# Optimization experiments

Measured on AMD Instinct MI355X. Metric: run time of the kernel, lower is better.

The kernel has to match this reference:

```python
import jax, jax.numpy as jnp
import numpy as np

S, D, H = 2048, 1024, 16
DH = D // H
EPS = 1e-5


def setup_inputs() -> dict:
    key = jax.random.key(0)
    ks = jax.random.split(key, 6)
    scale = 0.02
    return {
        "inputs": jax.random.normal(ks[0], (S, D), dtype=jnp.float32),
        "ln_w": jnp.ones((D,), dtype=jnp.float32),
        "ln_b": jnp.zeros((D,), dtype=jnp.float32),
        "Wq": jax.random.normal(ks[1], (D, D), dtype=jnp.float32) * scale,
        "Wk": jax.random.normal(ks[2], (D, D), dtype=jnp.float32) * scale,
        "Wv": jax.random.normal(ks[3], (D, D), dtype=jnp.float32) * scale,
        "Wo": jax.random.normal(ks[4], (D, D), dtype=jnp.float32) * scale,
    }


def reference(inputs, ln_w, ln_b, Wq, Wk, Wv, Wo):
    # Pre-LayerNorm (per token), matching eqx.nn.LayerNorm (eps=1e-5)
    mu = jnp.mean(inputs, axis=-1, keepdims=True)
    var = jnp.var(inputs, axis=-1, keepdims=True)
    x = (inputs - mu) / jnp.sqrt(var + EPS) * ln_w + ln_b  # [S, D]

    # QKV projections (eqx Linear: y = W @ x, no bias) -> [S, H, DH]
    q = (x @ Wq.T).reshape(S, H, DH)
    k = (x @ Wk.T).reshape(S, H, DH)
    v = (x @ Wv.T).reshape(S, H, DH)

    # Scaled dot-product attention; softmax forced to full precision
    scores = jnp.einsum("shd,thd->hst", q, k) / jnp.sqrt(jnp.asarray(DH, x.dtype))
    attn = jax.nn.softmax(scores.astype(jnp.float32), axis=-1).astype(x.dtype)
    # (dropout is identity in inference mode)
    ctx = jnp.einsum("hst,thd->shd", attn, v).reshape(S, D)

    out = ctx @ Wo.T  # output projection
    # outer dropout is identity in inference mode; residual add
    return out + inputs
```

## Files before the change

### kernel.cpp

```cpp
#include <hip/hip_runtime.h>
#include <cstdint>
#include <cstddef>

typedef unsigned short u16;
typedef unsigned int u32;
typedef __attribute__((ext_vector_type(8))) short bf16x8;
typedef __attribute__((ext_vector_type(4))) short bf16x4;
typedef __attribute__((ext_vector_type(4))) float f32x4;
typedef __attribute__((ext_vector_type(4))) unsigned short u16x4;

#if __has_builtin(__builtin_amdgcn_mfma_f32_16x16x16bf16_1k)
#define MFMA16(a, b, c) __builtin_amdgcn_mfma_f32_16x16x16bf16_1k(a, b, c, 0, 0, 0)
#else
static __device__ __forceinline__ f32x4 mfma16_asm(bf16x4 a, bf16x4 b, f32x4 c) {
  asm volatile("v_mfma_f32_16x16x16_bf16 %0, %1, %2, %0\n\ts_nop 4"
               : "+v"(c) : "v"(a), "v"(b));
  return c;
}
#define MFMA16(a, b, c) mfma16_asm(a, b, c)
#endif

#if __has_builtin(__builtin_amdgcn_exp2f)
#define EXP2(x) __builtin_amdgcn_exp2f(x)
#else
#define EXP2(x) exp2f(x)
#endif

#define WAITV(N) asm volatile("s_waitcnt vmcnt(" #N ")" ::: "memory")
#define MEMFENCE() asm volatile("" ::: "memory")

__device__ __forceinline__ u16 f2b(float f) {
  union { float f; unsigned u; } un; un.f = f;
  unsigned u = un.u;
  return (u16)((u + 0x7fffu + ((u >> 16) & 1u)) >> 16);
}

__device__ __forceinline__ u32 pkbf(float a, float b) {
  union { float f; u32 u; } ua, ub; ua.f = a; ub.f = b;
  return ((ua.u + 0x8000u) >> 16) | (((ub.u + 0x8000u) >> 16) << 16);
}

__device__ __forceinline__ void gload_lds16(const u16* g, u16* l) {
  __builtin_amdgcn_global_load_lds(
      (const __attribute__((address_space(1))) void*)g,
      (__attribute__((address_space(3))) void*)l, 16, 0, 0);
}

__device__ __forceinline__ void gemm128x128(
    const u16* __restrict__ A, const u16* __restrict__ B,
    u16* smA, u16* smB, int bm, int bn,
    float* outf, u16* outb, const float* __restrict__ resid, int ostride)
{
  const int tid = threadIdx.x;
  const int wave = tid >> 6, lane = tid & 63;
  const int quad = lane >> 4, l16 = lane & 15;
  const int wm = wave >> 1, wn = wave & 1;

  f32x4 acc[4][4];
  const f32x4 zero4 = {0.f, 0.f, 0.f, 0.f};
#pragma unroll
  for (int i = 0; i < 4; i++)
#pragma unroll
    for (int j = 0; j < 4; j++) acc[i][j] = zero4;

  const u16* Ab = A + (size_t)(bm * 128) * 1024;
  const u16* Bb = B + (size_t)(bn * 128) * 1024;

#define PSTAGE(buf, k0)                                                          \
  {                                                                              \
    _Pragma("unroll")                                                            \
    for (int i = 0; i < 4; i++) {                                                \
      const int idx = i * 256 + tid;                                             \
      const int row = idx >> 3, sl = idx & 7;                                    \
      const int g = (sl ^ (row & 7)) * 8;                                        \
      gload_lds16(Ab + (size_t)row * 1024 + (k0) + g,                            \
                  smA + (buf) * 8192 + (size_t)(i * 256 + wave * 64) * 8);       \
      gload_lds16(Bb + (size_t)row * 1024 + (k0) + g,                            \
                  smB + (buf) * 8192 + (size_t)(i * 256 + wave * 64) * 8);       \
    }                                                                            \
  }

  PSTAGE(0, 0);
  for (int t = 0; t < 16; t++) {
    const int cur = t & 1;
    if (t < 15) {
      PSTAGE(cur ^ 1, (t + 1) * 64);
      WAITV(8);
    } else {
      WAITV(0);
    }
    __builtin_amdgcn_s_barrier();
    const u16* sa = smA + cur * 8192;
    const u16* sb = smB + cur * 8192;
#pragma unroll
    for (int ks = 0; ks < 2; ks++) {
      const int swz = ((ks * 4 + quad) ^ (l16 & 7)) * 8;
      bf16x8 afr[4], bfr[4];
#pragma unroll
      for (int mt = 0; mt < 4; mt++)
        afr[mt] = *(const bf16x8*)(sa + (wm * 64 + mt * 16 + l16) * 64 + swz);
#pragma unroll
      for (int nt = 0; nt < 4; nt++)
        bfr[nt] = *(const bf16x8*)(sb + (wn * 64 + nt * 16 + l16) * 64 + swz);
      __builtin_amdgcn_s_setprio(1);
#pragma unroll
      for (int mt = 0; mt < 4; mt++)
#pragma unroll
        for (int nt = 0; nt < 4; nt++)
          acc[mt][nt] = __builtin_amdgcn_mfma_f32_16x16x32_bf16(afr[mt], bfr[nt], acc[mt][nt], 0, 0, 0);
      __builtin_amdgcn_s_setprio(0);
    }
    MEMFENCE();
    __builtin_amdgcn_s_barrier();
  }
#undef PSTAGE

#pragma unroll
  for (int mt = 0; mt < 4; mt++)
#pragma unroll
    for (int nt = 0; nt < 4; nt++)
#pragma unroll
      for (int r = 0; r < 4; r++) {
        const int row = bm * 128 + wm * 64 + mt * 16 + quad * 4 + r;
        const int col = bn * 128 + wn * 64 + nt * 16 + l16;
        if (outb) outb[(size_t)row * ostride + col] = f2b(acc[mt][nt][r]);
        else outf[(size_t)row * ostride + col] =
                 acc[mt][nt][r] + resid[(size_t)row * ostride + col];
      }
}

__global__ __launch_bounds__(256, 2) void proj_k(
    const u16* __restrict__ xb, const u16* __restrict__ Wb,
    u16* __restrict__ qkbuf, u16* __restrict__ vTb)
{
  __shared__ u16 smA[2 * 128 * 64];
  __shared__ u16 smB[2 * 128 * 64];
  int b = blockIdx.x;
  const u16 *A, *B; u16* o; int bm, bn;
  if (b < 256) {
    const int c = b & 7, i = b >> 3;
    bm = ((c >> 2) << 3) | (i & 7);
    bn = ((c & 3) << 2) | (i >> 3);
    A = xb; B = Wb; o = qkbuf;
  } else {
    b -= 256;
    const int c = b & 7, i = b >> 3;
    bm = i & 7;
    bn = (c << 1) | (i >> 3);
    A = Wb + (size_t)2 * (1 << 20); B = xb; o = vTb;
  }
  gemm128x128(A, B, smA, smB, bm, bn, nullptr, o, nullptr, 2048);
}

__global__ __launch_bounds__(256, 2) void out_k(
    const u16* __restrict__ ctxb, const u16* __restrict__ Wob,
    float* __restrict__ out, const float* __restrict__ x)
{
  __shared__ u16 smA[2 * 128 * 64];
  __shared__ u16 smB[2 * 128 * 64];
  const int b = blockIdx.x;
  const int c = b & 7, i = b >> 3;
  const int bm = ((c >> 2) << 3) | (i & 7);
  const int bn = ((c & 3) << 1) | (i >> 3);
  gemm128x128(ctxb, Wob, smA, smB, bm, bn, out, nullptr, x, 1024);
}

__global__ __launch_bounds__(256) void pre_k(
    const float* __restrict__ x, const float* __restrict__ lnw, const float* __restrict__ lnb,
    const float* __restrict__ w0, const float* __restrict__ w1,
    const float* __restrict__ w2, const float* __restrict__ w3,
    u16* __restrict__ xb, u16* __restrict__ Wb)
{
  const int b = blockIdx.x;
  const int tid = threadIdx.x;
  if (b < 2048) {
    const int s = b;
    const float4 v = ((const float4*)(x + (size_t)s * 1024))[tid];
    float sum = v.x + v.y + v.z + v.w;
    float sq  = v.x * v.x + v.y * v.y + v.z * v.z + v.w * v.w;
#pragma unroll
    for (int off = 32; off >= 1; off >>= 1) {
      sum += __shfl_down(sum, off);
      sq  += __shfl_down(sq, off);
    }
    __shared__ float sS[4], sQ[4];
    const int wave = tid >> 6, lane = tid & 63;
    if (lane == 0) { sS[wave] = sum; sQ[wave] = sq; }
    __syncthreads();
    const float ts = sS[0] + sS[1] + sS[2] + sS[3];
    const float tq = sQ[0] + sQ[1] + sQ[2] + sQ[3];
    const float mu = ts * (1.0f / 1024.0f);
    const float var = tq * (1.0f / 1024.0f) - mu * mu;
    const float rstd = rsqrtf(var + 1e-5f);
    const float4 wv = ((const float4*)lnw)[tid];
    const float4 bv = ((const float4*)lnb)[tid];
    u16x4 o;
    o[0] = f2b((v.x - mu) * rstd * wv.x + bv.x);
    o[1] = f2b((v.y - mu) * rstd * wv.y + bv.y);
    o[2] = f2b((v.z - mu) * rstd * wv.z + bv.z);
    o[3] = f2b((v.w - mu) * rstd * wv.w + bv.w);
    *(u16x4*)(xb + (size_t)s * 1024 + tid * 4) = o;
  } else {
    const unsigned i = (unsigned)(b - 2048) * 1024u + tid * 4u;
    const unsigned NW = 1u << 20;
    const float* src; unsigned loc; float sc;
    if (i < NW)            { src = w0; loc = i;           sc = 0.18033688f; }
    else if (i < 2u * NW)  { src = w1; loc = i - NW;      sc = 1.0f; }
    else if (i < 3u * NW)  { src = w2; loc = i - 2u * NW; sc = 1.0f; }
    else                   { src = w3; loc = i - 3u * NW; sc = 1.0f; }
    const float4 v = *(const float4*)(src + loc);
    u16x4 r;
    r[0] = f2b(v.x * sc); r[1] = f2b(v.y * sc); r[2] = f2b(v.z * sc); r[3] = f2b(v.w * sc);
    *(u16x4*)(Wb + i) = r;
  }
}

__global__ __launch_bounds__(256, 2) void attn_k(
    const u16* __restrict__ qkbuf,
    const u16* __restrict__ vT,
    u16* __restrict__ ctx)
{
  const int bid = blockIdx.x;
  const int work = (bid & 7) * 64 + (bid >> 3);
  const int h = work >> 5;
  const int q0 = (work & 31) * 64;
  __shared__ __align__(16) unsigned char arena[65536];
  u16* kvbuf = (u16*)arena;
  const int tid = threadIdx.x;
  const int wave = tid >> 6, lane = tid & 63;
  const int quad = lane >> 4, l16 = lane & 15;
  const int a7 = l16 & 7;
  const u16* kg = qkbuf + 1024;

  bf16x8 qf[4][2];
#pragma unroll
  for (int s = 0; s < 4; s++)
#pragma unroll
    for (int ks = 0; ks < 2; ks++)
      qf[s][ks] = *(const bf16x8*)(qkbuf + (size_t)(q0 + s * 16 + l16) * 2048 + h * 64 + ks * 32 + quad * 8);

  const f32x4 zero4 = {0.f, 0.f, 0.f, 0.f};
  f32x4 Oacc[4][4];
#pragma unroll
  for (int s = 0; s < 4; s++)
#pragma unroll
    for (int dt = 0; dt < 4; dt++) Oacc[s][dt] = zero4;
  float lacc[4] = {0.f, 0.f, 0.f, 0.f};

#define STAGE(T, bf)                                                                     \
  {                                                                                      \
    _Pragma("unroll")                                                                    \
    for (int i = 0; i < 4; i++) {                                                        \
      const int idx = (wave * 4 + i) * 64 + lane;                                        \
      const int kt = idx >> 3, kc = (idx & 7) ^ (kt & 7);                                \
      gload_lds16(kg + (size_t)((T) * 128 + kt) * 2048 + h * 64 + kc * 8,                \
                  kvbuf + (bf) * 16384 + (size_t)(wave * 4 + i) * 512);                  \
      const int vd = idx >> 4, vc = (idx & 15) ^ (vd & 7);                               \
      gload_lds16(vT + (size_t)(h * 64 + vd) * 2048 + (T) * 128 + vc * 8,                \
                  kvbuf + (bf) * 16384 + 8192 + (size_t)(wave * 4 + i) * 512);           \
    }                                                                                    \
  }

  STAGE(0, 0);

  for (int T = 0; T < 16; T++) {
    const int bf = T & 1;
    if (T + 1 < 16) {
      STAGE(T + 1, 1 - bf);
      WAITV(8);
    } else {
      WAITV(0);
    }
    __builtin_amdgcn_s_barrier();
    const u16* kb = kvbuf + bf * 16384;
    const u16* vb = kb + 8192;

    f32x4 st[2][4];
#pragma unroll
    for (int ntl = 0; ntl < 2; ntl++) {
      const int nt = wave * 2 + ntl;
      const u16* kr = kb + (nt * 16 + l16) * 64;
      const bf16x8 ka0 = *(const bf16x8*)(kr + (quad ^ a7) * 8);
      const bf16x8 ka1 = *(const bf16x8*)(kr + ((4 + quad) ^ a7) * 8);
      __builtin_amdgcn_s_setprio(1);
#pragma unroll
      for (int s = 0; s < 4; s++) {
        f32x4 t0 = __builtin_amdgcn_mfma_f32_16x16x32_bf16(ka0, qf[s][0], zero4, 0, 0, 0);
        st[ntl][s] = __builtin_amdgcn_mfma_f32_16x16x32_bf16(ka1, qf[s][1], t0, 0, 0, 0);
      }
      __builtin_amdgcn_s_setprio(0);
    }

    bf16x4 pk[2][4];
#pragma unroll
    for (int ntl = 0; ntl < 2; ntl++)
#pragma unroll
      for (int s = 0; s < 4; s++) {
        const float p0 = EXP2(st[ntl][s][0]);
        const float p1 = EXP2(st[ntl][s][1]);
        const float p2 = EXP2(st[ntl][s][2]);
        const float p3 = EXP2(st[ntl][s][3]);
        lacc[s] += (p0 + p1) + (p2 + p3);
        union { u32 u[2]; bf16x4 v; } pp;
        pp.u[0] = pkbf(p0, p1);
        pp.u[1] = pkbf(p2, p3);
        pk[ntl][s] = pp.v;
      }

#pragma unroll
    for (int ntl = 0; ntl < 2; ntl++)
#pragma unroll
      for (int dt = 0; dt < 4; dt++) {
        const bf16x4 bv = *(const bf16x4*)(vb + (dt * 16 + l16) * 128 +
            (((wave * 4 + ntl * 2 + (quad >> 1)) ^ a7) * 8 + (quad & 1) * 4));
        __builtin_amdgcn_s_setprio(1);
#pragma unroll
        for (int s = 0; s < 4; s++)
          Oacc[s][dt] = MFMA16(pk[ntl][s], bv, Oacc[s][dt]);
        __builtin_amdgcn_s_setprio(0);
      }
    MEMFENCE();
    __builtin_amdgcn_s_barrier();
  }
#undef STAGE

  float* rl = (float*)arena;
#pragma unroll
  for (int s = 0; s < 4; s++) {
    float l = lacc[s];
    l += __shfl_xor(l, 16);
    l += __shfl_xor(l, 32);
    if (quad == 0) rl[wave * 64 + s * 16 + l16] = l;
  }
  __syncthreads();
  const int m = tid >> 2, dg = (tid & 3) * 16;
  const float inv = 1.0f / (rl[m] + rl[64 + m] + rl[128 + m] + rl[192 + m]);
  __syncthreads();

  float* ro = (float*)arena;
#pragma unroll
  for (int s = 0; s < 4; s++)
#pragma unroll
    for (int dt = 0; dt < 4; dt++)
#pragma unroll
      for (int r = 0; r < 4; r++) {
        const int mr = s * 16 + quad * 4 + r;
        const int dc = (dt * 16 + l16) ^ ((mr & 7) << 1);
        ro[wave * 4096 + mr * 64 + dc] = Oacc[s][dt][r];
      }
  __syncthreads();
  u16* dst = ctx + (size_t)(q0 + m) * 1024 + h * 64 + dg;
  const int msw = (m & 7) << 1;
#pragma unroll
  for (int g = 0; g < 4; g++) {
    u16x4 o;
#pragma unroll
    for (int j = 0; j < 4; j++) {
      const int dc = (dg + g * 4 + j) ^ msw;
      const int base = m * 64 + dc;
      const float v = ro[base] + ro[4096 + base] + ro[8192 + base] + ro[12288 + base];
      o[j] = f2b(v * inv);
    }
    *(u16x4*)(dst + g * 4) = o;
  }
}

extern "C" void kernel_launch(void* const* d_in, const int* in_sizes, int n_in,
                              void* d_out, int out_size, void* d_ws, size_t ws_size,
                              hipStream_t stream)
{
  const float* x   = (const float*)d_in[0];
  const float* lnw = (const float*)d_in[1];
  const float* lnb = (const float*)d_in[2];
  const float* Wq  = (const float*)d_in[3];
  const float* Wk  = (const float*)d_in[4];
  const float* Wv  = (const float*)d_in[5];
  const float* Wo  = (const float*)d_in[6];

  u16* ws    = (u16*)d_ws;
  u16* xb    = ws;
  u16* Wb    = xb + (size_t)2048 * 1024;
  u16* qkbuf = Wb + (size_t)4 * 1024 * 1024;
  u16* vTb   = qkbuf + (size_t)2048 * 2048;
  u16* ctxb  = vTb + (size_t)1024 * 2048;

  pre_k<<<6144, 256, 0, stream>>>(x, lnw, lnb, Wq, Wk, Wv, Wo, xb, Wb);
  proj_k<<<384, 256, 0, stream>>>(xb, Wb, qkbuf, vTb);
  attn_k<<<512, 256, 0, stream>>>(qkbuf, vTb, ctxb);
  out_k<<<128, 256, 0, stream>>>(ctxb, Wb + (size_t)3 * (1 << 20), (float*)d_out, x);
}
```

Before: 153.1 us.

## Fuse four kernels into one persistent kernel with software grid barriers

```diff
diff --git a/kernel.cpp b/kernel.cpp
--- a/kernel.cpp
+++ b/kernel.cpp
@@ -8,6 +8,8 @@
 typedef __attribute__((ext_vector_type(4))) short bf16x4;
 typedef __attribute__((ext_vector_type(4))) float f32x4;
 typedef __attribute__((ext_vector_type(4))) unsigned short u16x4;
+
+#define NBLK 512
 
 #if __has_builtin(__builtin_amdgcn_mfma_f32_16x16x16bf16_1k)
 #define MFMA16(a, b, c) __builtin_amdgcn_mfma_f32_16x16x16bf16_1k(a, b, c, 0, 0, 0)
@@ -44,6 +46,27 @@
   __builtin_amdgcn_global_load_lds(
       (const __attribute__((address_space(1))) void*)g,
       (__attribute__((address_space(3))) void*)l, 16, 0, 0);
+}
+
+__device__ unsigned g_cnt[4] = {0, 0, 0, 0};
+__device__ unsigned g_gen[4] = {0, 0, 0, 0};
+
+__device__ __forceinline__ void gridbar(int i) {
+  __syncthreads();
+  if (threadIdx.x == 0) {
+    __threadfence();
+    unsigned g = __hip_atomic_load(&g_gen[i], __ATOMIC_RELAXED, __HIP_MEMORY_SCOPE_AGENT);
+    unsigned v = __hip_atomic_fetch_add(&g_cnt[i], 1u, __ATOMIC_ACQ_REL, __HIP_MEMORY_SCOPE_AGENT);
+    if (v == NBLK - 1u) {
+      __hip_atomic_store(&g_cnt[i], 0u, __ATOMIC_RELAXED, __HIP_MEMORY_SCOPE_AGENT);
+      __hip_atomic_fetch_add(&g_gen[i], 1u, __ATOMIC_RELEASE, __HIP_MEMORY_SCOPE_AGENT);
+    } else {
+      while (__hip_atomic_load(&g_gen[i], __ATOMIC_ACQUIRE, __HIP_MEMORY_SCOPE_AGENT) == g)
+        __builtin_amdgcn_s_sleep(2);
+    }
+    __threadfence();
+  }
+  __syncthreads();
 }
 
 __device__ __forceinline__ void gemm128x128(
@@ -129,123 +152,100 @@
       }
 }
 
-__global__ __launch_bounds__(256, 2) void proj_k(
-    const u16* __restrict__ xb, const u16* __restrict__ Wb,
-    u16* __restrict__ qkbuf, u16* __restrict__ vTb)
-{
-  __shared__ u16 smA[2 * 128 * 64];
-  __shared__ u16 smB[2 * 128 * 64];
-  int b = blockIdx.x;
-  const u16 *A, *B; u16* o; int bm, bn;
-  if (b < 256) {
-    const int c = b & 7, i = b >> 3;
-    bm = ((c >> 2) << 3) | (i & 7);
-    bn = ((c & 3) << 2) | (i >> 3);
-    A = xb; B = Wb; o = qkbuf;
-  } else {
-    b -= 256;
-    const int c = b & 7, i = b >> 3;
-    bm = i & 7;
-    bn = (c << 1) | (i >> 3);
-    A = Wb + (size_t)2 * (1 << 20); B = xb; o = vTb;
-  }
-  gemm128x128(A, B, smA, smB, bm, bn, nullptr, o, nullptr, 2048);
-}
-
-__global__ __launch_bounds__(256, 2) void out_k(
-    const u16* __restrict__ ctxb, const u16* __restrict__ Wob,
-    float* __restrict__ out, const float* __restrict__ x)
-{
-  __shared__ u16 smA[2 * 128 * 64];
-  __shared__ u16 smB[2 * 128 * 64];
-  const int b = blockIdx.x;
-  const int c = b & 7, i = b >> 3;
-  const int bm = ((c >> 2) << 3) | (i & 7);
-  const int bn = ((c & 3) << 1) | (i >> 3);
-  gemm128x128(ctxb, Wob, smA, smB, bm, bn, out, nullptr, x, 1024);
-}
-
-__global__ __launch_bounds__(256) void pre_k(
+__global__ __launch_bounds__(256, 2) void mega_k(
     const float* __restrict__ x, const float* __restrict__ lnw, const float* __restrict__ lnb,
     const float* __restrict__ w0, const float* __restrict__ w1,
     const float* __restrict__ w2, const float* __restrict__ w3,
-    u16* __restrict__ xb, u16* __restrict__ Wb)
+    u16* __restrict__ xb, u16* __restrict__ Wb,
+    u16* __restrict__ qkbuf, u16* __restrict__ vTb, u16* __restrict__ ctxb,
+    float* __restrict__ out)
 {
-  const int b = blockIdx.x;
+  __shared__ __align__(16) unsigned char arena[65536];
+  const int bid = blockIdx.x;
   const int tid = threadIdx.x;
-  if (b < 2048) {
-    const int s = b;
-    const float4 v = ((const float4*)(x + (size_t)s * 1024))[tid];
-    float sum = v.x + v.y + v.z + v.w;
-    float sq  = v.x * v.x + v.y * v.y + v.z * v.z + v.w * v.w;
-#pragma unroll
-    for (int off = 32; off >= 1; off >>= 1) {
-      sum += __shfl_down(sum, off);
-      sq  += __shfl_down(sq, off);
-    }
-    __shared__ float sS[4], sQ[4];
+
+  for (int u = bid; u < 6144; u += NBLK) {
+    if (u < 2048) {
+      const float4 v = ((const float4*)(x + (size_t)u * 1024))[tid];
+      float sum = v.x + v.y + v.z + v.w;
+      float sq  = v.x * v.x + v.y * v.y + v.z * v.z + v.w * v.w;
+#pragma unroll
+      for (int off = 32; off >= 1; off >>= 1) {
+        sum += __shfl_down(sum, off);
+        sq  += __shfl_down(sq, off);
+      }
+      float* sS = (float*)arena;
+      float* sQ = sS + 8;
+      const int wave = tid >> 6, lane = tid & 63;
+      __syncthreads();
+      if (lane == 0) { sS[wave] = sum; sQ[wave] = sq; }
+      __syncthreads();
+      const float ts = sS[0] + sS[1] + sS[2] + sS[3];
+      const float tq = sQ[0] + sQ[1] + sQ[2] + sQ[3];
+      const float mu = ts * (1.0f / 1024.0f);
+      const float var = tq * (1.0f / 1024.0f) - mu * mu;
+      const float rstd = rsqrtf(var + 1e-5f);
+      const float4 wv = ((const float4*)lnw)[tid];
+      const float4 bv = ((const float4*)lnb)[tid];
+      u16x4 o;
+      o[0] = f2b((v.x - mu) * rstd * wv.x + bv.x);
+      o[1] = f2b((v.y - mu) * rstd * wv.y + bv.y);
+      o[2] = f2b((v.z - mu) * rstd * wv.z + bv.z);
+      o[3] = f2b((v.w - mu) * rstd * wv.w + bv.w);
+      *(u16x4*)(xb + (size_t)u * 1024 + tid * 4) = o;
+    } else {
+      const unsigned i = (unsigned)(u - 2048) * 1024u + tid * 4u;
+      const unsigned NW = 1u << 20;
+      const float* src; unsigned loc; float sc;
+      if (i < NW)            { src = w0; loc = i;           sc = 0.18033688f; }
+      else if (i < 2u * NW)  { src = w1; loc = i - NW;      sc = 1.0f; }
+      else if (i < 3u * NW)  { src = w2; loc = i - 2u * NW; sc = 1.0f; }
+      else                   { src = w3; loc = i - 3u * NW; sc = 1.0f; }
+      const float4 v = *(const float4*)(src + loc);
+      u16x4 r;
+      r[0] = f2b(v.x * sc); r[1] = f2b(v.y * sc); r[2] = f2b(v.z * sc); r[3] = f2b(v.w * sc);
+      *(u16x4*)(Wb + i) = r;
+    }
+  }
+  gridbar(0);
+
+  if (bid < 384) {
+    u16* smA = (u16*)arena;
+    u16* smB = smA + 16384;
+    if (bid < 256) {
+      gemm128x128(xb, Wb, smA, smB, bid >> 4, bid & 15, nullptr, qkbuf, nullptr, 2048);
+    } else {
+      const int jj = bid - 256;
+      gemm128x128(Wb + (size_t)2 * (1 << 20), xb, smA, smB, jj >> 4, jj & 15,
+                  nullptr, vTb, nullptr, 2048);
+    }
+  }
+  gridbar(1);
+
+  {
+    const int work = (bid & 7) * 64 + (bid >> 3);
+    const int h = work >> 5;
+    const int q0 = (work & 31) * 64;
+    u16* kvbuf = (u16*)arena;
     const int wave = tid >> 6, lane = tid & 63;
-    if (lane == 0) { sS[wave] = sum; sQ[wave] = sq; }
-    __syncthreads();
-    const float ts = sS[0] + sS[1] + sS[2] + sS[3];
-    const float tq = sQ[0] + sQ[1] + sQ[2] + sQ[3];
-    const float mu = ts * (1.0f / 1024.0f);
-    const float var = tq * (1.0f / 1024.0f) - mu * mu;
-    const float rstd = rsqrtf(var + 1e-5f);
-    const float4 wv = ((const float4*)lnw)[tid];
-    const float4 bv = ((const float4*)lnb)[tid];
-    u16x4 o;
-    o[0] = f2b((v.x - mu) * rstd * wv.x + bv.x);
-    o[1] = f2b((v.y - mu) * rstd * wv.y + bv.y);
-    o[2] = f2b((v.z - mu) * rstd * wv.z + bv.z);
-    o[3] = f2b((v.w - mu) * rstd * wv.w + bv.w);
-    *(u16x4*)(xb + (size_t)s * 1024 + tid * 4) = o;
-  } else {
-    const unsigned i = (unsigned)(b - 2048) * 1024u + tid * 4u;
-    const unsigned NW = 1u << 20;
-    const float* src; unsigned loc; float sc;
-    if (i < NW)            { src = w0; loc = i;           sc = 0.18033688f; }
-    else if (i < 2u * NW)  { src = w1; loc = i - NW;      sc = 1.0f; }
-    else if (i < 3u * NW)  { src = w2; loc = i - 2u * NW; sc = 1.0f; }
-    else                   { src = w3; loc = i - 3u * NW; sc = 1.0f; }
-    const float4 v = *(const float4*)(src + loc);
-    u16x4 r;
-    r[0] = f2b(v.x * sc); r[1] = f2b(v.y * sc); r[2] = f2b(v.z * sc); r[3] = f2b(v.w * sc);
-    *(u16x4*)(Wb + i) = r;
-  }
-}
-
-__global__ __launch_bounds__(256, 2) void attn_k(
-    const u16* __restrict__ qkbuf,
-    const u16* __restrict__ vT,
-    u16* __restrict__ ctx)
-{
-  const int bid = blockIdx.x;
-  const int work = (bid & 7) * 64 + (bid >> 3);
-  const int h = work >> 5;
-  const int q0 = (work & 31) * 64;
-  __shared__ __align__(16) unsigned char arena[65536];
-  u16* kvbuf = (u16*)arena;
-  const int tid = threadIdx.x;
-  const int wave = tid >> 6, lane = tid & 63;
-  const int quad = lane >> 4, l16 = lane & 15;
-  const int a7 = l16 & 7;
-  const u16* kg = qkbuf + 1024;
-
-  bf16x8 qf[4][2];
-#pragma unroll
-  for (int s = 0; s < 4; s++)
-#pragma unroll
-    for (int ks = 0; ks < 2; ks++)
-      qf[s][ks] = *(const bf16x8*)(qkbuf + (size_t)(q0 + s * 16 + l16) * 2048 + h * 64 + ks * 32 + quad * 8);
-
-  const f32x4 zero4 = {0.f, 0.f, 0.f, 0.f};
-  f32x4 Oacc[4][4];
-#pragma unroll
-  for (int s = 0; s < 4; s++)
-#pragma unroll
-    for (int dt = 0; dt < 4; dt++) Oacc[s][dt] = zero4;
-  float lacc[4] = {0.f, 0.f, 0.f, 0.f};
+    const int quad = lane >> 4, l16 = lane & 15;
+    const int a7 = l16 & 7;
+    const u16* kg = qkbuf + 1024;
+
+    bf16x8 qf[4][2];
+#pragma unroll
+    for (int s = 0; s < 4; s++)
+#pragma unroll
+      for (int ks = 0; ks < 2; ks++)
+        qf[s][ks] = *(const bf16x8*)(qkbuf + (size_t)(q0 + s * 16 + l16) * 2048 + h * 64 + ks * 32 + quad * 8);
+
+    const f32x4 zero4 = {0.f, 0.f, 0.f, 0.f};
+    f32x4 Oacc[4][4];
+#pragma unroll
+    for (int s = 0; s < 4; s++)
+#pragma unroll
+      for (int dt = 0; dt < 4; dt++) Oacc[s][dt] = zero4;
+    float lacc[4] = {0.f, 0.f, 0.f, 0.f};
 
 #define STAGE(T, bf)                                                                     \
   {                                                                                      \
@@ -260,108 +260,118 @@
                   kvbuf + (bf) * 16384 + 8192 + (size_t)(wave * 4 + i) * 512);           \
     }                                                                                    \
   }
-
-  STAGE(0, 0);
-
-  for (int T = 0; T < 16; T++) {
-    const int bf = T & 1;
-    if (T + 1 < 16) {
-      STAGE(T + 1, 1 - bf);
-      WAITV(8);
-    } else {
-      WAITV(0);
-    }
-    __builtin_amdgcn_s_barrier();
-    const u16* kb = kvbuf + bf * 16384;
-    const u16* vb = kb + 8192;
-
-    f32x4 st[2][4];
-#pragma unroll
-    for (int ntl = 0; ntl < 2; ntl++) {
-      const int nt = wave * 2 + ntl;
-      const u16* kr = kb + (nt * 16 + l16) * 64;
-      const bf16x8 ka0 = *(const bf16x8*)(kr + (quad ^ a7) * 8);
-      const bf16x8 ka1 = *(const bf16x8*)(kr + ((4 + quad) ^ a7) * 8);
-      __builtin_amdgcn_s_setprio(1);
-#pragma unroll
-      for (int s = 0; s < 4; s++) {
-        f32x4 t0 = __builtin_amdgcn_mfma_f32_16x16x32_bf16(ka0, qf[s][0], zero4, 0, 0, 0);
-        st[ntl][s] = __builtin_amdgcn_mfma_f32_16x16x32_bf16(ka1, qf[s][1], t0, 0, 0, 0);
-      }
-      __builtin_amdgcn_s_setprio(0);
-    }
-
-    bf16x4 pk[2][4];
-#pragma unroll
-    for (int ntl = 0; ntl < 2; ntl++)
-#pragma unroll
-      for (int s = 0; s < 4; s++) {
-        const float p0 = EXP2(st[ntl][s][0]);
-        const float p1 = EXP2(st[ntl][s][1]);
-        const float p2 = EXP2(st[ntl][s][2]);
-        const float p3 = EXP2(st[ntl][s][3]);
-        lacc[s] += (p0 + p1) + (p2 + p3);
-        union { u32 u[2]; bf16x4 v; } pp;
-        pp.u[0] = pkbf(p0, p1);
-        pp.u[1] = pkbf(p2, p3);
-        pk[ntl][s] = pp.v;
-      }
-
-#pragma unroll
-    for (int ntl = 0; ntl < 2; ntl++)
-#pragma unroll
-      for (int dt = 0; dt < 4; dt++) {
-        const bf16x4 bv = *(const bf16x4*)(vb + (dt * 16 + l16) * 128 +
-            (((wave * 4 + ntl * 2 + (quad >> 1)) ^ a7) * 8 + (quad & 1) * 4));
+#define vT vTb
+    STAGE(0, 0);
+
+    for (int T = 0; T < 16; T++) {
+      const int bf = T & 1;
+      if (T + 1 < 16) {
+        STAGE(T + 1, 1 - bf);
+        WAITV(8);
+      } else {
+        WAITV(0);
+      }
+      __builtin_amdgcn_s_barrier();
+      const u16* kb = kvbuf + bf * 16384;
+      const u16* vb = kb + 8192;
+
+      f32x4 st[2][4];
+#pragma unroll
+      for (int ntl = 0; ntl < 2; ntl++) {
+        const int nt = wave * 2 + ntl;
+        const u16* kr = kb + (nt * 16 + l16) * 64;
+        const bf16x8 ka0 = *(const bf16x8*)(kr + (quad ^ a7) * 8);
+        const bf16x8 ka1 = *(const bf16x8*)(kr + ((4 + quad) ^ a7) * 8);
         __builtin_amdgcn_s_setprio(1);
 #pragma unroll
-        for (int s = 0; s < 4; s++)
-          Oacc[s][dt] = MFMA16(pk[ntl][s], bv, Oacc[s][dt]);
+        for (int s = 0; s < 4; s++) {
+          f32x4 t0 = __builtin_amdgcn_mfma_f32_16x16x32_bf16(ka0, qf[s][0], zero4, 0, 0, 0);
+          st[ntl][s] = __builtin_amdgcn_mfma_f32_16x16x32_bf16(ka1, qf[s][1], t0, 0, 0, 0);
+        }
         __builtin_amdgcn_s_setprio(0);
       }
-    MEMFENCE();
-    __builtin_amdgcn_s_barrier();
-  }
+
+      bf16x4 pk[2][4];
+#pragma unroll
+      for (int ntl = 0; ntl < 2; ntl++)
+#pragma unroll
+        for (int s = 0; s < 4; s++) {
+          const float p0 = EXP2(st[ntl][s][0]);
+          const float p1 = EXP2(st[ntl][s][1]);
+          const float p2 = EXP2(st[ntl][s][2]);
+          const float p3 = EXP2(st[ntl][s][3]);
+          lacc[s] += (p0 + p1) + (p2 + p3);
+          union { u32 u[2]; bf16x4 v; } pp;
+          pp.u[0] = pkbf(p0, p1);
+          pp.u[1] = pkbf(p2, p3);
+          pk[ntl][s] = pp.v;
+        }
+
+#pragma unroll
+      for (int ntl = 0; ntl < 2; ntl++)
+#pragma unroll
+        for (int dt = 0; dt < 4; dt++) {
+          const bf16x4 bv = *(const bf16x4*)(vb + (dt * 16 + l16) * 128 +
+              (((wave * 4 + ntl * 2 + (quad >> 1)) ^ a7) * 8 + (quad & 1) * 4));
+          __builtin_amdgcn_s_setprio(1);
+#pragma unroll
+          for (int s = 0; s < 4; s++)
+            Oacc[s][dt] = MFMA16(pk[ntl][s], bv, Oacc[s][dt]);
+          __builtin_amdgcn_s_setprio(0);
+        }
+      MEMFENCE();
+      __builtin_amdgcn_s_barrier();
+    }
 #undef STAGE
-
-  float* rl = (float*)arena;
-#pragma unroll
-  for (int s = 0; s < 4; s++) {
-    float l = lacc[s];
-    l += __shfl_xor(l, 16);
-    l += __shfl_xor(l, 32);
-    if (quad == 0) rl[wave * 64 + s * 16 + l16] = l;
-  }
-  __syncthreads();
-  const int m = tid >> 2, dg = (tid & 3) * 16;
-  const float inv = 1.0f / (rl[m] + rl[64 + m] + rl[128 + m] + rl[192 + m]);
-  __syncthreads();
-
-  float* ro = (float*)arena;
-#pragma unroll
-  for (int s = 0; s < 4; s++)
-#pragma unroll
-    for (int dt = 0; dt < 4; dt++)
-#pragma unroll
-      for (int r = 0; r < 4; r++) {
-        const int mr = s * 16 + quad * 4 + r;
-        const int dc = (dt * 16 + l16) ^ ((mr & 7) << 1);
-        ro[wave * 4096 + mr * 64 + dc] = Oacc[s][dt][r];
-      }
-  __syncthreads();
-  u16* dst = ctx + (size_t)(q0 + m) * 1024 + h * 64 + dg;
-  const int msw = (m & 7) << 1;
-#pragma unroll
-  for (int g = 0; g < 4; g++) {
-    u16x4 o;
-#pragma unroll
-    for (int j = 0; j < 4; j++) {
-      const int dc = (dg + g * 4 + j) ^ msw;
-      const int base = m * 64 + dc;
-      const float v = ro[base] + ro[4096 + base] + ro[8192 + base] + ro[12288 + base];
-      o[j] = f2b(v * inv);
-    }
-    *(u16x4*)(dst + g * 4) = o;
+#undef vT
+
+    float* rl = (float*)arena;
+#pragma unroll
+    for (int s = 0; s < 4; s++) {
+      float l = lacc[s];
+      l += __shfl_xor(l, 16);
+      l += __shfl_xor(l, 32);
+      if (quad == 0) rl[wave * 64 + s * 16 + l16] = l;
+    }
+    __syncthreads();
+    const int m = tid >> 2, dg = (tid & 3) * 16;
+    const float inv = 1.0f / (rl[m] + rl[64 + m] + rl[128 + m] + rl[192 + m]);
+    __syncthreads();
+
+    float* ro = (float*)arena;
+#pragma unroll
+    for (int s = 0; s < 4; s++)
+#pragma unroll
+      for (int dt = 0; dt < 4; dt++)
+#pragma unroll
+        for (int r = 0; r < 4; r++) {
+          const int mr = s * 16 + quad * 4 + r;
+          const int dc = (dt * 16 + l16) ^ ((mr & 7) << 1);
+          ro[wave * 4096 + mr * 64 + dc] = Oacc[s][dt][r];
+        }
+    __syncthreads();
+    u16* dst = ctxb + (size_t)(q0 + m) * 1024 + h * 64 + dg;
+    const int msw = (m & 7) << 1;
+#pragma unroll
+    for (int g = 0; g < 4; g++) {
+      u16x4 o;
+#pragma unroll
+      for (int j = 0; j < 4; j++) {
+        const int dc = (dg + g * 4 + j) ^ msw;
+        const int base = m * 64 + dc;
+        const float v = ro[base] + ro[4096 + base] + ro[8192 + base] + ro[12288 + base];
+        o[j] = f2b(v * inv);
+      }
+      *(u16x4*)(dst + g * 4) = o;
+    }
+  }
+  gridbar(2);
+
+  if (bid < 128) {
+    u16* smA = (u16*)arena;
+    u16* smB = smA + 16384;
+    gemm128x128(ctxb, Wb + (size_t)3 * (1 << 20), smA, smB, bid >> 3, bid & 7,
+                out, nullptr, x, 1024);
   }
 }
 
@@ -384,8 +394,6 @@
   u16* vTb   = qkbuf + (size_t)2048 * 2048;
   u16* ctxb  = vTb + (size_t)1024 * 2048;
 
-  pre_k<<<6144, 256, 0, stream>>>(x, lnw, lnb, Wq, Wk, Wv, Wo, xb, Wb);
-  proj_k<<<384, 256, 0, stream>>>(xb, Wb, qkbuf, vTb);
-  attn_k<<<512, 256, 0, stream>>>(qkbuf, vTb, ctxb);
-  out_k<<<128, 256, 0, stream>>>(ctxb, Wb + (size_t)3 * (1 << 20), (float*)d_out, x);
-}
+  mega_k<<<NBLK, 256, 0, stream>>>(x, lnw, lnb, Wq, Wk, Wv, Wo,
+                                   xb, Wb, qkbuf, vTb, ctxb, (float*)d_out);
+}
```

New measurement: 370.3 us. 2.42x slower.
